# Kernel tuning notes

Hardware: AMD Instinct MI355X
Metric: run time of the kernel (lower is better)

## Reference

```python
import jax, jax.numpy as jnp
import numpy as np
from jax import lax

B, C, H, W = 16, 3, 256, 256
K = 3          # lbp kernel size (odd)
POOL = 2
Q = 8          # quant_len
LN_EPS = 1e-5


def _lbp_kernel(c, k):
    half = k // 2
    idx_pairs = [[[0, 0], [k - 1, k - 1]],
                 [[0, half], [k - 1, half]],
                 [[0, k - 1], [k - 1, 0]],
                 [[half, k - 1], [half, 0]]]
    kerns = []
    for pair in idx_pairs:
        for idx in pair:
            m = np.zeros((c, k, k), np.float32)
            m[:, half, half] = 1.0
            m[:, idx[0], idx[1]] = -1.0
            kerns.append(m)
    return jnp.asarray(np.stack(kerns))  # [8, C, K, K]


LBP_KERNEL = _lbp_kernel(C, K)


def setup_inputs() -> dict:
    key = jax.random.key(0)
    ks = jax.random.split(key, 8)
    return {
        "x": jax.random.normal(ks[0], (B, C, H, W), jnp.float32),
        "clamp_low": jnp.float32(-150.0),
        "clamp_high": jnp.float32(150.0),
        "w_expand": jax.random.normal(ks[1], (56, 3, 1, 1), jnp.float32) * 0.1,
        "b_expand": jax.random.normal(ks[2], (56,), jnp.float32) * 0.05,
        "w_conv": jax.random.normal(ks[3], (16, 4, 1, 1), jnp.float32) * 0.1,
        "b_conv": jax.random.normal(ks[4], (16,), jnp.float32) * 0.05,
        "w_final": jax.random.normal(ks[5], (1, 16, 3, 3), jnp.float32) * 0.1,
        "b_final": jax.random.normal(ks[6], (1,), jnp.float32) * 0.05,
    }


def reference(x, clamp_low, clamp_high, w_expand, b_expand, w_conv, b_conv, w_final, b_final):
    leaky = lambda v: jax.nn.leaky_relu(v, 0.01)
    bsz = x.shape[0]

    # avg_pool2d(kernel=POOL, stride=1, pad=POOL//2, count_include_pad=True) -> [B,C,H+1,W+1]
    pad = POOL // 2
    xp = lax.reduce_window(x, 0.0, lax.add, (1, 1, POOL, POOL), (1, 1, 1, 1),
                           [(0, 0), (0, 0), (pad, pad), (pad, pad)]) / float(POOL * POOL)

    # LBP difference conv: 8 output channels, SAME padding
    hk = K // 2
    xl = lax.conv_general_dilated(xp, LBP_KERNEL, (1, 1), [(hk, hk), (hk, hk)],
                                  dimension_numbers=("NCHW", "OIHW", "NCHW"))
    xl = jnp.clip(xl, clamp_low, clamp_high)

    b4 = bsz * 4
    hp, wp = xl.shape[-2], xl.shape[-1]
    n = hp * wp
    xl = xl.reshape(b4, 2, n)  # [B4, 2, N]

    # per-sample, per-channel quantization boundaries: measure[b,i,c] = i*cd + min
    mn = xl.min(axis=-1)                       # [B4, 2]
    mx = xl.max(axis=-1)                       # [B4, 2]
    cd = (mx - mn) / Q
    measure = jnp.arange(Q + 1, dtype=xl.dtype)[None, :, None] * cd[:, None, :] + mn[:, None, :]  # [B4,Q+1,2]

    def bin_mask(vals, ch):
        # keep raw value where lo_i <= v <= hi_i, else 0  -> [B4, Q, N]
        v = vals[:, None, :]
        lo = measure[:, :-1, ch][:, :, None]
        hi = measure[:, 1:, ch][:, :, None]
        return jnp.where((v >= lo) & (v <= hi), v, 0.0)

    m0 = bin_mask(xl[:, 0, :], 0)  # [B4, Q, N]
    m1 = bin_mask(xl[:, 1, :], 1)  # [B4, Q, N]

    # joint histogram of masked values: equivalent to per-pixel outer product + one-hot mask conv
    hist = jnp.einsum("bin,bjn->bij", m0, m1)       # [B4, Q, Q]
    hist = hist / jnp.sum(hist)                      # global normalizer (torch.sum(x))
    hist = hist.reshape(b4, Q * Q, 1)

    # levels: (bin_index + 1) * measure[:, 1, :]
    ii, jj = jnp.meshgrid(jnp.arange(Q), jnp.arange(Q), indexing="ij")
    idxs = jnp.stack([ii, jj], axis=-1).reshape(Q * Q, 2)          # cartesian_prod order
    levels = (idxs[None].astype(xl.dtype) + 1.0) * measure[:, 1, :][:, None, :]  # [B4,64,2]

    feat = jnp.concatenate([levels, hist], axis=2)   # [B4, 64, 3]
    feat = feat.reshape(bsz, 4, Q * Q, 3).transpose(0, 3, 1, 2)  # [B, 3, 4, 64]

    # 1x1 conv 3 -> 56
    h = leaky(jnp.einsum("bcij,oc->boij", feat, w_expand[:, :, 0, 0]) + b_expand[None, :, None, None])
    h = h.transpose(0, 2, 3, 1)  # [B, 4, 64, 56] -> channels=4, spatial (64,56)

    # nearest interpolate spatial (64,56) -> (H,W): src = floor(dst * in / out)
    src_h = (jnp.arange(H) * h.shape[2]) // H
    src_w = (jnp.arange(W) * h.shape[3]) // W
    h = h[:, :, src_h][:, :, :, src_w]  # [B, 4, H, W]

    # layer_norm over last two dims, no affine
    mean = h.mean(axis=(-2, -1), keepdims=True)
    var = jnp.mean((h - mean) ** 2, axis=(-2, -1), keepdims=True)
    h = (h - mean) / jnp.sqrt(var + LN_EPS)

    # 1x1 conv 4 -> 16
    h = leaky(jnp.einsum("bchw,oc->bohw", h, w_conv[:, :, 0, 0]) + b_conv[None, :, None, None])

    # 3x3 conv 16 -> 1, SAME padding
    out = lax.conv_general_dilated(h, w_final, (1, 1), [(1, 1), (1, 1)],
                                   dimension_numbers=("NCHW", "OIHW", "NCHW"))
    out = leaky(out + b_final[None, :, None, None])
    return out
```

## Files before the change

kernel.cpp:

```cpp
#include <hip/hip_runtime.h>
#include <stdint.h>
#include <math.h>

#define HH 256
#define WW 256
#define BATCH 16
#define HP 257
#define SROW 264
#define SH 259
#define SBP (SH*SROW)
#define NPART 32


__device__ __forceinline__ float leaky(float v){ return v >= 0.f ? v : 0.01f*v; }

__device__ __forceinline__ void group_off(int k, int& dh, int& dw){
    dh = (k == 3) ? 0 : -1;
    dw = (k == 3) ? 1 : (k - 1);
}

__global__ __launch_bounds__(256) void k1(const float* __restrict__ x, float* __restrict__ s,
                                          float* __restrict__ pmn, float* __restrict__ pmx,
                                          float* __restrict__ hist){
    __shared__ __align__(16) float xs[12][264];
    __shared__ __align__(16) float ps[11][264];
    __shared__ float redmn[4][8], redmx[4][8];
    int c = blockIdx.x, b = blockIdx.y;
    int tid = threadIdx.x, wv = tid >> 6, lane = tid & 63;
    int h0 = c*8;
    int nr = (c == 31) ? 9 : 8;

    if (c == 0 && b == 0){
        for (int t = tid; t < 4096; t += 256) hist[t] = 0.f;
    }
    float* sb = s + (size_t)b*SBP;
    for (int t = tid; t < nr*7; t += 256){
        int rr = t/7, k = t%7;
        int col = (k < 4) ? k : (257 + k);
        sb[(size_t)(h0+1+rr)*SROW + col] = 0.f;
    }
    if (c == 0){  for (int t = tid; t < SROW; t += 256) sb[t] = 0.f; }
    if (c == 31){ for (int t = tid; t < SROW; t += 256) sb[(size_t)258*SROW + t] = 0.f; }

    const float* xb = x + (size_t)b*3*HH*WW;
    for (int t = tid; t < 12*66; t += 256){
        int i = t/66, q = t - i*66;
        int r = h0 - 2 + i;
        float4 v = make_float4(0.f, 0.f, 0.f, 0.f);
        if (q >= 1 && q <= 64 && (unsigned)r < 256u){
            const float* base = xb + (size_t)r*WW + (q-1)*4;
            float4 a = *(const float4*)(base);
            float4 d = *(const float4*)(base + HH*WW);
            float4 e = *(const float4*)(base + 2*HH*WW);
            v.x = a.x + d.x + e.x;
            v.y = a.y + d.y + e.y;
            v.z = a.z + d.z + e.z;
            v.w = a.w + d.w + e.w;
        }
        *(float4*)&xs[i][q*4] = v;
    }
    __syncthreads();

    int np = (nr+2)*257;
    for (int t = tid; t < np; t += 256){
        int j = t/257, w = t - j*257;
        int h = h0 - 1 + j;
        float v = 0.f;
        if ((unsigned)h < (unsigned)HP)
            v = 0.25f*(xs[j][w+3] + xs[j][w+4] + xs[j+1][w+3] + xs[j+1][w+4]);
        ps[j][w+4] = v;
    }
    for (int t = tid; t < (nr+2)*7; t += 256){
        int j = t/7, k = t%7;
        ps[j][(k < 4) ? k : (257 + k)] = 0.f;
    }
    __syncthreads();

    float mn[8], mx[8];
    #pragma unroll
    for (int q=0;q<8;q++){ mn[q]=INFINITY; mx[q]=-INFINITY; }
    int nd = nr*257;
    for (int t = tid; t < nd; t += 256){
        int lr = t/257, w = t - lr*257;
        int h = h0 + lr;
        float cv = ps[lr+1][w+4];
        sb[(size_t)(h+1)*SROW + (w+4)] = cv;
        float d;
        d = cv - ps[lr  ][w+3]; mn[0]=fminf(mn[0],d); mx[0]=fmaxf(mx[0],d);
        d = cv - ps[lr+2][w+5]; mn[1]=fminf(mn[1],d); mx[1]=fmaxf(mx[1],d);
        d = cv - ps[lr  ][w+4]; mn[2]=fminf(mn[2],d); mx[2]=fmaxf(mx[2],d);
        d = cv - ps[lr+2][w+4]; mn[3]=fminf(mn[3],d); mx[3]=fmaxf(mx[3],d);
        d = cv - ps[lr  ][w+5]; mn[4]=fminf(mn[4],d); mx[4]=fmaxf(mx[4],d);
        d = cv - ps[lr+2][w+3]; mn[5]=fminf(mn[5],d); mx[5]=fmaxf(mx[5],d);
        d = cv - ps[lr+1][w+5]; mn[6]=fminf(mn[6],d); mx[6]=fmaxf(mx[6],d);
        d = cv - ps[lr+1][w+3]; mn[7]=fminf(mn[7],d); mx[7]=fmaxf(mx[7],d);
    }
    #pragma unroll
    for (int off=32; off; off>>=1){
        #pragma unroll
        for (int q=0;q<8;q++){
            mn[q] = fminf(mn[q], __shfl_down(mn[q], off));
            mx[q] = fmaxf(mx[q], __shfl_down(mx[q], off));
        }
    }
    if (lane == 0){
        #pragma unroll
        for (int q=0;q<8;q++){ redmn[wv][q]=mn[q]; redmx[wv][q]=mx[q]; }
    }
    __syncthreads();
    int blk = b*NPART + c;
    if (tid < 8){
        pmn[(size_t)blk*8 + tid] = fminf(fminf(redmn[0][tid],redmn[1][tid]),
                                         fminf(redmn[2][tid],redmn[3][tid]));
        pmx[(size_t)blk*8 + tid] = fmaxf(fmaxf(redmx[0][tid],redmx[1][tid]),
                                         fmaxf(redmx[2][tid],redmx[3][tid]));
    }
}

__global__ __launch_bounds__(256) void k2(const float* __restrict__ s, const float* __restrict__ cl,
                                          const float* __restrict__ chp,
                                          const float* __restrict__ pmn, const float* __restrict__ pmx,
                                          float* __restrict__ hist){
    __shared__ __align__(16) float lh[4*64*32];
    __shared__ __align__(16) float band[7][264];
    int c = blockIdx.x, b = blockIdx.y;
    int tid = threadIdx.x, wv = tid >> 6, lane = tid & 63;
    int h0 = c*4;
    int nr = (c == 63) ? 5 : 4;

    float4 z4 = make_float4(0.f,0.f,0.f,0.f);
    float4* lhv = (float4*)lh;
    for (int t = tid; t < 2048; t += 256) lhv[t] = z4;

    const float* sb = s + (size_t)b*SBP;
    int tot = (nr+2)*66;
    for (int t = tid; t < tot; t += 256){
        int lr = t/66, q = t - lr*66;
        *(float4*)&band[lr][q*4] = *(const float4*)(sb + (size_t)(h0+lr)*SROW + q*4);
    }

    float mnA=INFINITY, mxA=-INFINITY, mnB=INFINITY, mxB=-INFINITY;
    for (int t = lane; t < NPART; t += 64){
        const float* pn = pmn + ((size_t)(b*NPART + t))*8;
        const float* px = pmx + ((size_t)(b*NPART + t))*8;
        mnA = fminf(mnA, pn[2*wv]);   mxA = fmaxf(mxA, px[2*wv]);
        mnB = fminf(mnB, pn[2*wv+1]); mxB = fmaxf(mxB, px[2*wv+1]);
    }
    #pragma unroll
    for (int off=32; off; off>>=1){
        mnA = fminf(mnA, __shfl_down(mnA, off)); mxA = fmaxf(mxA, __shfl_down(mxA, off));
        mnB = fminf(mnB, __shfl_down(mnB, off)); mxB = fmaxf(mxB, __shfl_down(mxB, off));
    }
    mnA = __shfl(mnA, 0); mxA = __shfl(mxA, 0);
    mnB = __shfl(mnB, 0); mxB = __shfl(mxB, 0);
    float lo = cl[0], hi = chp[0];
    float mn0 = fminf(fmaxf(mnA, lo), hi), mx0 = fminf(fmaxf(mxA, lo), hi);
    float mn1 = fminf(fmaxf(mnB, lo), hi), mx1 = fminf(fmaxf(mxB, lo), hi);
    float cd0 = (mx0-mn0)*0.125f;
    float cd1 = (mx1-mn1)*0.125f;
    float m0[9], m1[9];
    #pragma unroll
    for (int i=0;i<9;i++){
        m0[i] = __fadd_rn(__fmul_rn((float)i, cd0), mn0);
        m1[i] = __fadd_rn(__fmul_rn((float)i, cd1), mn1);
    }
    int g = b*4 + wv;
    int dh, dw; group_off(wv, dh, dw);
    float* lhg = lh + wv*2048 + (lane & 31);
    __syncthreads();

    int npx = nr*257;
    for (int p = lane; p < npx; p += 64){
        int lrr = p/257;
        int w = p - lrr*257;
        float cc = band[lrr+1][w+4];
        float v0 = fminf(fmaxf(cc - band[lrr+1+dh][w+4+dw], lo), hi);
        float v1 = fminf(fmaxf(cc - band[lrr+1-dh][w+4-dw], lo), hi);
        unsigned b0=0, b1=0;
        #pragma unroll
        for (int i=0;i<8;i++){
            b0 |= (v0>=m0[i] && v0<=m0[i+1]) ? (1u<<i) : 0u;
            b1 |= (v1>=m1[i] && v1<=m1[i+1]) ? (1u<<i) : 0u;
        }
        float pr = v0*v1;
        unsigned bb0=b0;
        while (bb0){
            int i = __ffs(bb0)-1; bb0 &= bb0-1;
            unsigned bb1=b1;
            while (bb1){
                int j = __ffs(bb1)-1; bb1 &= bb1-1;
                atomicAdd(&lhg[(i*8+j)*32], pr);
            }
        }
    }
    __syncthreads();
    float acc = 0.f;
    #pragma unroll
    for (int r=0;r<32;r++) acc += lh[(wv*64 + lane)*32 + ((lane + r)&31)];
    if (acc != 0.f) atomicAdd(&hist[g*64 + lane], acc);
}

__global__ __launch_bounds__(256) void k3(const float* __restrict__ hist,
                    const float* __restrict__ pmn, const float* __restrict__ pmx,
                    const float* __restrict__ cl, const float* __restrict__ chp,
                    const float* __restrict__ we, const float* __restrict__ be,
                    const float* __restrict__ wc, const float* __restrict__ bc,
                    const float* __restrict__ wf, const float* __restrict__ bf,
                    float* __restrict__ out){
    __shared__ float hloc[4*3584];
    __shared__ float w9l[4*9*56];
    __shared__ float wfl[144];
    __shared__ float wred[4][16];
    __shared__ float gmn[8], gmx[8];
    __shared__ float gstat[8];
    __shared__ float sred[4];
    int ch = blockIdx.x, b = blockIdx.y;
    int tid = threadIdx.x, wv = tid >> 6, lane = tid & 63;
    if (tid < 144) wfl[tid] = wf[tid];

    float rmn[8], rmx[8];
    #pragma unroll
    for (int q=0;q<8;q++){ rmn[q]=INFINITY; rmx[q]=-INFINITY; }
    for (int t = tid; t < NPART; t += 256){
        const float* pn = pmn + ((size_t)(b*NPART + t))*8;
        const float* px = pmx + ((size_t)(b*NPART + t))*8;
        #pragma unroll
        for (int q=0;q<8;q++){ rmn[q]=fminf(rmn[q],pn[q]); rmx[q]=fmaxf(rmx[q],px[q]); }
    }
    #pragma unroll
    for (int off=32; off; off>>=1){
        #pragma unroll
        for (int q=0;q<8;q++){
            rmn[q] = fminf(rmn[q], __shfl_down(rmn[q], off));
            rmx[q] = fmaxf(rmx[q], __shfl_down(rmx[q], off));
        }
    }
    if (lane == 0){
        #pragma unroll
        for (int q=0;q<8;q++){ wred[wv][q]=rmn[q]; wred[wv][8+q]=rmx[q]; }
    }
    __syncthreads();
    if (tid < 8)
        gmn[tid] = fminf(fminf(wred[0][tid],wred[1][tid]), fminf(wred[2][tid],wred[3][tid]));
    else if (tid < 16){
        int q = tid-8;
        gmx[q] = fmaxf(fmaxf(wred[0][8+q],wred[1][8+q]), fmaxf(wred[2][8+q],wred[3][8+q]));
    }

    float ps = 0.f;
    for (int t = tid; t < 4096; t += 256) ps += hist[t];
    #pragma unroll
    for (int off=32; off; off>>=1) ps += __shfl_down(ps, off);
    if (lane == 0) sred[wv] = ps;
    __syncthreads();
    float S = sred[0]+sred[1]+sred[2]+sred[3];

    int g = b*4 + wv;
    float lo = cl[0], hi = chp[0];
    float mn0 = fminf(fmaxf(gmn[2*wv  ], lo), hi), mx0 = fminf(fmaxf(gmx[2*wv  ], lo), hi);
    float mn1 = fminf(fmaxf(gmn[2*wv+1], lo), hi), mx1 = fminf(fmaxf(gmx[2*wv+1], lo), hi);
    float lvl0 = __fadd_rn(__fmul_rn(1.0f,(mx0-mn0)*0.125f), mn0);
    float lvl1 = __fadd_rn(__fmul_rn(1.0f,(mx1-mn1)*0.125f), mn1);
    for (int e = lane; e < 3584; e += 64){
        int ij = e/56, o = e - ij*56;
        int i = ij>>3, j = ij&7;
        float f0 = __fmul_rn((float)(i+1), lvl0);
        float f1 = __fmul_rn((float)(j+1), lvl1);
        float f2 = hist[g*64+ij] / S;
        float a = f0*we[o*3+0] + f1*we[o*3+1] + f2*we[o*3+2] + be[o];
        hloc[wv*3584 + e] = leaky(a);
    }
    float pm = 0.f;
    for (int e = lane; e < 3584; e += 64){
        int o = e%56;
        int lo_ = (32*o+6)/7, hi_ = (32*o+31)/7;
        pm += hloc[wv*3584+e] * (float)(4*(hi_-lo_+1));
    }
    #pragma unroll
    for (int off=32; off; off>>=1) pm += __shfl_down(pm, off);
    pm = __shfl(pm, 0);
    float mean = pm * (1.0f/65536.0f);
    float pv = 0.f;
    for (int e = lane; e < 3584; e += 64){
        int o = e%56;
        int lo_ = (32*o+6)/7, hi_ = (32*o+31)/7;
        float d = hloc[wv*3584+e] - mean;
        pv += d*d * (float)(4*(hi_-lo_+1));
    }
    #pragma unroll
    for (int off=32; off; off>>=1) pv += __shfl_down(pv, off);
    pv = __shfl(pv, 0);
    if (lane == 0){
        gstat[wv*2+0] = mean;
        gstat[wv*2+1] = 1.0f / sqrtf(pv * (1.0f/65536.0f) + 1e-5f);
    }
    __syncthreads();

    int rm = (2*ch-1 > 0) ? (2*ch-1) : 0;
    int rp = (2*ch+2 < 63) ? (2*ch+2) : 63;
    int ne = (rp-rm+1)*56;
    for (int e = tid; e < ne; e += 256){
        int rr = e/56, sxc = e - rr*56;
        int eg = (rm+rr)*56 + sxc;
        float hn[4];
        #pragma unroll
        for (int k=0;k<4;k++) hn[k] = (hloc[k*3584+eg] - gstat[2*k]) * gstat[2*k+1];
        float w9v[9] = {0,0,0,0,0,0,0,0,0};
        #pragma unroll
        for (int c2=0;c2<16;c2++){
            float hv = bc[c2];
            #pragma unroll
            for (int k=0;k<4;k++) hv += wc[c2*4+k]*hn[k];
            hv = leaky(hv);
            #pragma unroll
            for (int t=0;t<9;t++) w9v[t] += wfl[c2*9+t]*hv;
        }
        #pragma unroll
        for (int t=0;t<9;t++) w9l[rr*504 + t*56 + sxc] = w9v[t];
    }
    __syncthreads();

    float bf0 = bf[0];
    int x = tid;
    int sxm = ((x-1)*7) >> 5;
    int sx0 = (x*7) >> 5;
    int sxp = ((x+1)*7) >> 5;
    for (int yo=0; yo<8; ++yo){
        int y = ch*8 + yo;
        float acc = bf0;
        #pragma unroll
        for (int dy=0; dy<3; ++dy){
            int yy = y + dy - 1;
            if ((unsigned)yy >= 256u) continue;
            const float* wr = &w9l[((yy>>2) - rm)*504 + dy*3*56];
            if (x >= 1)   acc += wr[sxm];
                          acc += wr[56 + sx0];
            if (x <= 254) acc += wr[2*56 + sxp];
        }
        out[((size_t)(b*256 + y))*256 + x] = leaky(acc);
    }
}

extern "C" void kernel_launch(void* const* d_in, const int* in_sizes, int n_in,
                              void* d_out, int out_size, void* d_ws, size_t ws_size,
                              hipStream_t stream){
    const float* x  = (const float*)d_in[0];
    const float* cl = (const float*)d_in[1];
    const float* ch = (const float*)d_in[2];
    const float* we = (const float*)d_in[3];
    const float* be = (const float*)d_in[4];
    const float* wc = (const float*)d_in[5];
    const float* bc = (const float*)d_in[6];
    const float* wf = (const float*)d_in[7];
    const float* bf = (const float*)d_in[8];
    float* out = (float*)d_out;

    float* s = (float*)d_ws;
    size_t off = (size_t)BATCH*SBP;
    float* pmn  = s + off; off += (size_t)BATCH*NPART*8;
    float* pmx  = s + off; off += (size_t)BATCH*NPART*8;
    float* hist = s + off; off += 4096;

    k1<<<dim3(32,BATCH), 256, 0, stream>>>(x, s, pmn, pmx, hist);
    k2<<<dim3(64,BATCH), 256, 0, stream>>>(s, cl, ch, pmn, pmx, hist);
    k3<<<dim3(32,BATCH), 256, 0, stream>>>(hist, pmn, pmx, cl, ch, we, be, wc, bc, wf, bf, out);
}
```

Measured before the change: 149.0 us.

## Halve band height in k1/k3 and recompute expand activations instead of storing in LDS

The first and third kernels now process 4-row bands, doubling their grid to 64 blocks per image so the GPU has more parallel work. Kernel 3 no longer holds the full 4x3584 expand activation array in shared memory. It keeps only the normalized 4x64 histogram and recomputes each activation on demand, which cuts LDS use and allows the new launch bounds of 4 blocks per CU. The cost is redundant recomputation of the expand layer and of the per-image statistics in every block, with twice as many blocks doing that work.

```diff
diff --git a/kernel.cpp b/kernel.cpp
--- a/kernel.cpp
+++ b/kernel.cpp
@@ -9,7 +9,8 @@
 #define SROW 264
 #define SH 259
 #define SBP (SH*SROW)
-#define NPART 32
+#define NBAND 64
+#define NPART 64
 
 
 __device__ __forceinline__ float leaky(float v){ return v >= 0.f ? v : 0.01f*v; }
@@ -19,16 +20,27 @@
     dw = (k == 3) ? 1 : (k - 1);
 }
 
-__global__ __launch_bounds__(256) void k1(const float* __restrict__ x, float* __restrict__ s,
-                                          float* __restrict__ pmn, float* __restrict__ pmx,
-                                          float* __restrict__ hist){
-    __shared__ __align__(16) float xs[12][264];
-    __shared__ __align__(16) float ps[11][264];
+__device__ __forceinline__ float expand_a(int ij, int o, float lvl0, float lvl1,
+                                          const float* hh_g,
+                                          const float* __restrict__ we,
+                                          const float* __restrict__ be){
+    int i = ij>>3, j = ij&7;
+    float f0 = __fmul_rn((float)(i+1), lvl0);
+    float f1 = __fmul_rn((float)(j+1), lvl1);
+    float f2 = hh_g[ij];
+    return leaky(f0*we[o*3+0] + f1*we[o*3+1] + f2*we[o*3+2] + be[o]);
+}
+
+__global__ __launch_bounds__(256, 4) void ka(const float* __restrict__ x, float* __restrict__ s,
+                                             float* __restrict__ pmn, float* __restrict__ pmx,
+                                             float* __restrict__ hist){
+    __shared__ __align__(16) float xs[8][264];
+    __shared__ __align__(16) float ps[7][264];
     __shared__ float redmn[4][8], redmx[4][8];
     int c = blockIdx.x, b = blockIdx.y;
     int tid = threadIdx.x, wv = tid >> 6, lane = tid & 63;
-    int h0 = c*8;
-    int nr = (c == 31) ? 9 : 8;
+    int h0 = c*4;
+    int nr = (c == NBAND-1) ? 5 : 4;
 
     if (c == 0 && b == 0){
         for (int t = tid; t < 4096; t += 256) hist[t] = 0.f;
@@ -39,11 +51,12 @@
         int col = (k < 4) ? k : (257 + k);
         sb[(size_t)(h0+1+rr)*SROW + col] = 0.f;
     }
-    if (c == 0){  for (int t = tid; t < SROW; t += 256) sb[t] = 0.f; }
-    if (c == 31){ for (int t = tid; t < SROW; t += 256) sb[(size_t)258*SROW + t] = 0.f; }
+    if (c == 0){        for (int t = tid; t < SROW; t += 256) sb[t] = 0.f; }
+    if (c == NBAND-1){  for (int t = tid; t < SROW; t += 256) sb[(size_t)258*SROW + t] = 0.f; }
 
     const float* xb = x + (size_t)b*3*HH*WW;
-    for (int t = tid; t < 12*66; t += 256){
+    int nxr = nr + 3;
+    for (int t = tid; t < nxr*66; t += 256){
         int i = t/66, q = t - i*66;
         int r = h0 - 2 + i;
         float4 v = make_float4(0.f, 0.f, 0.f, 0.f);
@@ -117,16 +130,16 @@
     }
 }
 
-__global__ __launch_bounds__(256) void k2(const float* __restrict__ s, const float* __restrict__ cl,
-                                          const float* __restrict__ chp,
-                                          const float* __restrict__ pmn, const float* __restrict__ pmx,
-                                          float* __restrict__ hist){
+__global__ __launch_bounds__(256, 4) void kb(const float* __restrict__ s, const float* __restrict__ cl,
+                                             const float* __restrict__ chp,
+                                             const float* __restrict__ pmn, const float* __restrict__ pmx,
+                                             float* __restrict__ hist){
     __shared__ __align__(16) float lh[4*64*32];
     __shared__ __align__(16) float band[7][264];
     int c = blockIdx.x, b = blockIdx.y;
     int tid = threadIdx.x, wv = tid >> 6, lane = tid & 63;
     int h0 = c*4;
-    int nr = (c == 63) ? 5 : 4;
+    int nr = (c == NBAND-1) ? 5 : 4;
 
     float4 z4 = make_float4(0.f,0.f,0.f,0.f);
     float4* lhv = (float4*)lh;
@@ -200,19 +213,20 @@
     if (acc != 0.f) atomicAdd(&hist[g*64 + lane], acc);
 }
 
-__global__ __launch_bounds__(256) void k3(const float* __restrict__ hist,
+__global__ __launch_bounds__(256, 4) void kc(const float* __restrict__ hist,
                     const float* __restrict__ pmn, const float* __restrict__ pmx,
                     const float* __restrict__ cl, const float* __restrict__ chp,
                     const float* __restrict__ we, const float* __restrict__ be,
                     const float* __restrict__ wc, const float* __restrict__ bc,
                     const float* __restrict__ wf, const float* __restrict__ bf,
                     float* __restrict__ out){
-    __shared__ float hloc[4*3584];
-    __shared__ float w9l[4*9*56];
+    __shared__ float hh[4][64];
+    __shared__ float w9l[3*9*56];
     __shared__ float wfl[144];
     __shared__ float wred[4][16];
     __shared__ float gmn[8], gmx[8];
     __shared__ float gstat[8];
+    __shared__ float glvl[8];
     __shared__ float sred[4];
     int ch = blockIdx.x, b = blockIdx.y;
     int tid = threadIdx.x, wv = tid >> 6, lane = tid & 63;
@@ -239,42 +253,38 @@
         #pragma unroll
         for (int q=0;q<8;q++){ wred[wv][q]=rmn[q]; wred[wv][8+q]=rmx[q]; }
     }
-    __syncthreads();
+    float ps = 0.f;
+    for (int t = tid; t < 4096; t += 256) ps += hist[t];
+    #pragma unroll
+    for (int off=32; off; off>>=1) ps += __shfl_down(ps, off);
+    if (lane == 0) sred[wv] = ps;
+    __syncthreads();
+
     if (tid < 8)
         gmn[tid] = fminf(fminf(wred[0][tid],wred[1][tid]), fminf(wred[2][tid],wred[3][tid]));
     else if (tid < 16){
         int q = tid-8;
         gmx[q] = fmaxf(fmaxf(wred[0][8+q],wred[1][8+q]), fmaxf(wred[2][8+q],wred[3][8+q]));
     }
-
-    float ps = 0.f;
-    for (int t = tid; t < 4096; t += 256) ps += hist[t];
-    #pragma unroll
-    for (int off=32; off; off>>=1) ps += __shfl_down(ps, off);
-    if (lane == 0) sred[wv] = ps;
-    __syncthreads();
     float S = sred[0]+sred[1]+sred[2]+sred[3];
-
-    int g = b*4 + wv;
+    for (int t = tid; t < 256; t += 256)
+        hh[t>>6][t&63] = hist[b*256 + t] / S;
+    __syncthreads();
+
     float lo = cl[0], hi = chp[0];
     float mn0 = fminf(fmaxf(gmn[2*wv  ], lo), hi), mx0 = fminf(fmaxf(gmx[2*wv  ], lo), hi);
     float mn1 = fminf(fmaxf(gmn[2*wv+1], lo), hi), mx1 = fminf(fmaxf(gmx[2*wv+1], lo), hi);
     float lvl0 = __fadd_rn(__fmul_rn(1.0f,(mx0-mn0)*0.125f), mn0);
     float lvl1 = __fadd_rn(__fmul_rn(1.0f,(mx1-mn1)*0.125f), mn1);
+    if (lane == 0){ glvl[2*wv] = lvl0; glvl[2*wv+1] = lvl1; }
+
+    const float* hhg = hh[wv];
+    float pm = 0.f;
     for (int e = lane; e < 3584; e += 64){
         int ij = e/56, o = e - ij*56;
-        int i = ij>>3, j = ij&7;
-        float f0 = __fmul_rn((float)(i+1), lvl0);
-        float f1 = __fmul_rn((float)(j+1), lvl1);
-        float f2 = hist[g*64+ij] / S;
-        float a = f0*we[o*3+0] + f1*we[o*3+1] + f2*we[o*3+2] + be[o];
-        hloc[wv*3584 + e] = leaky(a);
-    }
-    float pm = 0.f;
-    for (int e = lane; e < 3584; e += 64){
-        int o = e%56;
+        float a = expand_a(ij, o, lvl0, lvl1, hhg, we, be);
         int lo_ = (32*o+6)/7, hi_ = (32*o+31)/7;
-        pm += hloc[wv*3584+e] * (float)(4*(hi_-lo_+1));
+        pm += a * (float)(4*(hi_-lo_+1));
     }
     #pragma unroll
     for (int off=32; off; off>>=1) pm += __shfl_down(pm, off);
@@ -282,9 +292,10 @@
     float mean = pm * (1.0f/65536.0f);
     float pv = 0.f;
     for (int e = lane; e < 3584; e += 64){
-        int o = e%56;
+        int ij = e/56, o = e - ij*56;
+        float a = expand_a(ij, o, lvl0, lvl1, hhg, we, be);
         int lo_ = (32*o+6)/7, hi_ = (32*o+31)/7;
-        float d = hloc[wv*3584+e] - mean;
+        float d = a - mean;
         pv += d*d * (float)(4*(hi_-lo_+1));
     }
     #pragma unroll
@@ -296,15 +307,18 @@
     }
     __syncthreads();
 
-    int rm = (2*ch-1 > 0) ? (2*ch-1) : 0;
-    int rp = (2*ch+2 < 63) ? (2*ch+2) : 63;
+    int rm = (ch-1 > 0) ? (ch-1) : 0;
+    int rp = (ch+1 < 63) ? (ch+1) : 63;
     int ne = (rp-rm+1)*56;
     for (int e = tid; e < ne; e += 256){
         int rr = e/56, sxc = e - rr*56;
-        int eg = (rm+rr)*56 + sxc;
+        int ij = rm + rr;
         float hn[4];
         #pragma unroll
-        for (int k=0;k<4;k++) hn[k] = (hloc[k*3584+eg] - gstat[2*k]) * gstat[2*k+1];
+        for (int k=0;k<4;k++){
+            float a = expand_a(ij, sxc, glvl[2*k], glvl[2*k+1], hh[k], we, be);
+            hn[k] = (a - gstat[2*k]) * gstat[2*k+1];
+        }
         float w9v[9] = {0,0,0,0,0,0,0,0,0};
         #pragma unroll
         for (int c2=0;c2<16;c2++){
@@ -325,8 +339,8 @@
     int sxm = ((x-1)*7) >> 5;
     int sx0 = (x*7) >> 5;
     int sxp = ((x+1)*7) >> 5;
-    for (int yo=0; yo<8; ++yo){
-        int y = ch*8 + yo;
+    for (int yo=0; yo<4; ++yo){
+        int y = ch*4 + yo;
         float acc = bf0;
         #pragma unroll
         for (int dy=0; dy<3; ++dy){
@@ -361,7 +375,7 @@
     float* pmx  = s + off; off += (size_t)BATCH*NPART*8;
     float* hist = s + off; off += 4096;
 
-    k1<<<dim3(32,BATCH), 256, 0, stream>>>(x, s, pmn, pmx, hist);
-    k2<<<dim3(64,BATCH), 256, 0, stream>>>(s, cl, ch, pmn, pmx, hist);
-    k3<<<dim3(32,BATCH), 256, 0, stream>>>(hist, pmn, pmx, cl, ch, we, be, wc, bc, wf, bf, out);
-}
+    ka<<<dim3(NBAND,BATCH), 256, 0, stream>>>(x, s, pmn, pmx, hist);
+    kb<<<dim3(NBAND,BATCH), 256, 0, stream>>>(s, cl, ch, pmn, pmx, hist);
+    kc<<<dim3(NBAND,BATCH), 256, 0, stream>>>(hist, pmn, pmx, cl, ch, we, be, wc, bc, wf, bf, out);
+}
```

After: 220.2 us. 1.48x slower.

## Split k3 into per-batch stats kernel and conv kernel, recompute expand on the fly

Applied to the files above, without the earlier changes.

The redundant per-block computation of the expanded feature map and its layer-norm statistics (previously repeated in all 32 row-chunk blocks per batch) moves into a small per-batch kernel that writes levels, normalized histogram and mean/rstd to workspace. The conv kernel reads these stats and recomputes only the needed expand values for its rows, and the 57KB hloc shared buffer goes away, which should allow higher occupancy. The cost is an extra kernel launch and a serial dependency, and the per-batch kernel runs only 16 blocks.

```diff
diff --git a/kernel.cpp b/kernel.cpp
--- a/kernel.cpp
+++ b/kernel.cpp
@@ -10,6 +10,7 @@
 #define SH 259
 #define SBP (SH*SROW)
 #define NPART 32
+#define NSTAT 272
 
 
 __device__ __forceinline__ float leaky(float v){ return v >= 0.f ? v : 0.01f*v; }
@@ -17,6 +18,17 @@
 __device__ __forceinline__ void group_off(int k, int& dh, int& dw){
     dh = (k == 3) ? 0 : -1;
     dw = (k == 3) ? 1 : (k - 1);
+}
+
+__device__ __forceinline__ float expand_a(int ij, int o, float lvl0, float lvl1,
+                                          const float* hh_g,
+                                          const float* __restrict__ we,
+                                          const float* __restrict__ be){
+    int i = ij>>3, j = ij&7;
+    float f0 = __fmul_rn((float)(i+1), lvl0);
+    float f1 = __fmul_rn((float)(j+1), lvl1);
+    float f2 = hh_g[ij];
+    return leaky(f0*we[o*3+0] + f1*we[o*3+1] + f2*we[o*3+2] + be[o]);
 }
 
 __global__ __launch_bounds__(256) void k1(const float* __restrict__ x, float* __restrict__ s,
@@ -200,23 +212,19 @@
     if (acc != 0.f) atomicAdd(&hist[g*64 + lane], acc);
 }
 
-__global__ __launch_bounds__(256) void k3(const float* __restrict__ hist,
+__global__ __launch_bounds__(256) void kpre(const float* __restrict__ hist,
                     const float* __restrict__ pmn, const float* __restrict__ pmx,
                     const float* __restrict__ cl, const float* __restrict__ chp,
                     const float* __restrict__ we, const float* __restrict__ be,
-                    const float* __restrict__ wc, const float* __restrict__ bc,
-                    const float* __restrict__ wf, const float* __restrict__ bf,
-                    float* __restrict__ out){
-    __shared__ float hloc[4*3584];
-    __shared__ float w9l[4*9*56];
-    __shared__ float wfl[144];
+                    float* __restrict__ stats){
     __shared__ float wred[4][16];
     __shared__ float gmn[8], gmx[8];
     __shared__ float gstat[8];
+    __shared__ float glvl[8];
     __shared__ float sred[4];
-    int ch = blockIdx.x, b = blockIdx.y;
+    __shared__ float hh[4][64];
+    int b = blockIdx.x;
     int tid = threadIdx.x, wv = tid >> 6, lane = tid & 63;
-    if (tid < 144) wfl[tid] = wf[tid];
 
     float rmn[8], rmx[8];
     #pragma unroll
@@ -239,42 +247,38 @@
         #pragma unroll
         for (int q=0;q<8;q++){ wred[wv][q]=rmn[q]; wred[wv][8+q]=rmx[q]; }
     }
-    __syncthreads();
+    float ps = 0.f;
+    for (int t = tid; t < 4096; t += 256) ps += hist[t];
+    #pragma unroll
+    for (int off=32; off; off>>=1) ps += __shfl_down(ps, off);
+    if (lane == 0) sred[wv] = ps;
+    __syncthreads();
+
     if (tid < 8)
         gmn[tid] = fminf(fminf(wred[0][tid],wred[1][tid]), fminf(wred[2][tid],wred[3][tid]));
     else if (tid < 16){
         int q = tid-8;
         gmx[q] = fmaxf(fmaxf(wred[0][8+q],wred[1][8+q]), fmaxf(wred[2][8+q],wred[3][8+q]));
     }
-
-    float ps = 0.f;
-    for (int t = tid; t < 4096; t += 256) ps += hist[t];
-    #pragma unroll
-    for (int off=32; off; off>>=1) ps += __shfl_down(ps, off);
-    if (lane == 0) sred[wv] = ps;
-    __syncthreads();
     float S = sred[0]+sred[1]+sred[2]+sred[3];
-
-    int g = b*4 + wv;
+    for (int t = tid; t < 256; t += 256)
+        hh[t>>6][t&63] = hist[b*256 + t] / S;
+    __syncthreads();
+
     float lo = cl[0], hi = chp[0];
     float mn0 = fminf(fmaxf(gmn[2*wv  ], lo), hi), mx0 = fminf(fmaxf(gmx[2*wv  ], lo), hi);
     float mn1 = fminf(fmaxf(gmn[2*wv+1], lo), hi), mx1 = fminf(fmaxf(gmx[2*wv+1], lo), hi);
     float lvl0 = __fadd_rn(__fmul_rn(1.0f,(mx0-mn0)*0.125f), mn0);
     float lvl1 = __fadd_rn(__fmul_rn(1.0f,(mx1-mn1)*0.125f), mn1);
+    if (lane == 0){ glvl[2*wv] = lvl0; glvl[2*wv+1] = lvl1; }
+
+    const float* hhg = hh[wv];
+    float pm = 0.f;
     for (int e = lane; e < 3584; e += 64){
         int ij = e/56, o = e - ij*56;
-        int i = ij>>3, j = ij&7;
-        float f0 = __fmul_rn((float)(i+1), lvl0);
-        float f1 = __fmul_rn((float)(j+1), lvl1);
-        float f2 = hist[g*64+ij] / S;
-        float a = f0*we[o*3+0] + f1*we[o*3+1] + f2*we[o*3+2] + be[o];
-        hloc[wv*3584 + e] = leaky(a);
-    }
-    float pm = 0.f;
-    for (int e = lane; e < 3584; e += 64){
-        int o = e%56;
+        float a = expand_a(ij, o, lvl0, lvl1, hhg, we, be);
         int lo_ = (32*o+6)/7, hi_ = (32*o+31)/7;
-        pm += hloc[wv*3584+e] * (float)(4*(hi_-lo_+1));
+        pm += a * (float)(4*(hi_-lo_+1));
     }
     #pragma unroll
     for (int off=32; off; off>>=1) pm += __shfl_down(pm, off);
@@ -282,9 +286,10 @@
     float mean = pm * (1.0f/65536.0f);
     float pv = 0.f;
     for (int e = lane; e < 3584; e += 64){
-        int o = e%56;
+        int ij = e/56, o = e - ij*56;
+        float a = expand_a(ij, o, lvl0, lvl1, hhg, we, be);
         int lo_ = (32*o+6)/7, hi_ = (32*o+31)/7;
-        float d = hloc[wv*3584+e] - mean;
+        float d = a - mean;
         pv += d*d * (float)(4*(hi_-lo_+1));
     }
     #pragma unroll
@@ -296,15 +301,51 @@
     }
     __syncthreads();
 
+    float* st = stats + (size_t)b*NSTAT;
+    for (int t = tid; t < NSTAT; t += 256){
+        float v;
+        if (t < 8)        v = glvl[t];
+        else if (t < 16)  v = gstat[t-8];
+        else              v = hh[(t-16)>>6][(t-16)&63];
+        st[t] = v;
+    }
+}
+
+__global__ __launch_bounds__(256) void kcp(const float* __restrict__ stats,
+                    const float* __restrict__ we, const float* __restrict__ be,
+                    const float* __restrict__ wc, const float* __restrict__ bc,
+                    const float* __restrict__ wf, const float* __restrict__ bf,
+                    float* __restrict__ out){
+    __shared__ float hh[4][64];
+    __shared__ float glvl[8];
+    __shared__ float gstat[8];
+    __shared__ float w9l[4*9*56];
+    __shared__ float wfl[144];
+    int ch = blockIdx.x, b = blockIdx.y;
+    int tid = threadIdx.x;
+    if (tid < 144) wfl[tid] = wf[tid];
+
+    const float* st = stats + (size_t)b*NSTAT;
+    for (int t = tid; t < NSTAT; t += 256){
+        float v = st[t];
+        if (t < 8)        glvl[t] = v;
+        else if (t < 16)  gstat[t-8] = v;
+        else              hh[(t-16)>>6][(t-16)&63] = v;
+    }
+    __syncthreads();
+
     int rm = (2*ch-1 > 0) ? (2*ch-1) : 0;
     int rp = (2*ch+2 < 63) ? (2*ch+2) : 63;
     int ne = (rp-rm+1)*56;
     for (int e = tid; e < ne; e += 256){
         int rr = e/56, sxc = e - rr*56;
-        int eg = (rm+rr)*56 + sxc;
+        int ij = rm + rr;
         float hn[4];
         #pragma unroll
-        for (int k=0;k<4;k++) hn[k] = (hloc[k*3584+eg] - gstat[2*k]) * gstat[2*k+1];
+        for (int k=0;k<4;k++){
+            float a = expand_a(ij, sxc, glvl[2*k], glvl[2*k+1], hh[k], we, be);
+            hn[k] = (a - gstat[2*k]) * gstat[2*k+1];
+        }
         float w9v[9] = {0,0,0,0,0,0,0,0,0};
         #pragma unroll
         for (int c2=0;c2<16;c2++){
@@ -357,11 +398,13 @@
 
     float* s = (float*)d_ws;
     size_t off = (size_t)BATCH*SBP;
-    float* pmn  = s + off; off += (size_t)BATCH*NPART*8;
-    float* pmx  = s + off; off += (size_t)BATCH*NPART*8;
-    float* hist = s + off; off += 4096;
+    float* pmn   = s + off; off += (size_t)BATCH*NPART*8;
+    float* pmx   = s + off; off += (size_t)BATCH*NPART*8;
+    float* hist  = s + off; off += 4096;
+    float* stats = s + off; off += (size_t)BATCH*NSTAT;
 
     k1<<<dim3(32,BATCH), 256, 0, stream>>>(x, s, pmn, pmx, hist);
     k2<<<dim3(64,BATCH), 256, 0, stream>>>(s, cl, ch, pmn, pmx, hist);
-    k3<<<dim3(32,BATCH), 256, 0, stream>>>(hist, pmn, pmx, cl, ch, we, be, wc, bc, wf, bf, out);
-}
+    kpre<<<BATCH, 256, 0, stream>>>(hist, pmn, pmx, cl, ch, we, be, stats);
+    kcp<<<dim3(32,BATCH), 256, 0, stream>>>(stats, we, be, wc, bc, wf, bf, out);
+}
```

After: 150.4 us. Within noise of the previous version (+1.0%).
